# Performance work log

Hardware: AMD Instinct MI355X
Metric: run time of the kernel (lower is better)

Reference implementation:

```python
import jax, jax.numpy as jnp
import numpy as np

K = 16  # neighbors

def setup_inputs() -> dict:
    key = jax.random.key(0)
    x = jax.random.normal(key, (2, 8192, 64), dtype=jnp.float32)
    return {"x": x}

def reference(x):
    # pairwise squared euclidean distance: ||xi||^2 - 2 xi.xj + ||xj||^2
    b, n, d = x.shape
    x_inner = -2.0 * jnp.einsum('bnd,bmd->bnm', x, x)          # (B,N,N)
    x_sq = jnp.sum(x * x, axis=-1, keepdims=True)               # (B,N,1)
    dist = x_sq + x_inner + jnp.swapaxes(x_sq, 1, 2)            # (B,N,N)
    # torch.topk(-dist, k) -> largest of -dist == k nearest neighbors
    _, nn_idx = jax.lax.top_k(-dist, K)                         # (B,N,K) int32
    center_idx = jnp.broadcast_to(jnp.arange(n, dtype=nn_idx.dtype)[None, :, None], (b, n, K))
    return jnp.stack((nn_idx, center_idx), axis=0)              # (2,B,N,K)
```

## Files before the change

### kernel.cpp

```cpp
#include <hip/hip_runtime.h>
#include <stdint.h>

constexpr int N_    = 8192;
constexpr int D_    = 64;
constexpr int K_    = 16;
constexpr int NQ    = 16384;
constexpr int MS    = 8;
constexpr int CAPB  = 40;

typedef __attribute__((ext_vector_type(8))) short bf16x8;
typedef __attribute__((ext_vector_type(4))) float f32x4;

template<int JN>
__device__ __forceinline__ void topk_insertf(float (&key)[JN], float nk) {
    if (nk < key[JN - 1]) {
        bool c[JN];
#pragma unroll
        for (int j = 0; j < JN; ++j) c[j] = nk < key[j];
#pragma unroll
        for (int j = JN - 1; j >= 1; --j)
            key[j] = c[j - 1] ? key[j - 1] : (c[j] ? nk : key[j]);
        key[0] = c[0] ? nk : key[0];
    }
}

__device__ __forceinline__ unsigned short bf16_rne(float f) {
    uint32_t u = __float_as_uint(f);
    return (unsigned short)((u + 0x7FFFu + ((u >> 16) & 1u)) >> 16);
}

__global__ void __launch_bounds__(256) split_k(const float* __restrict__ x,
                                               unsigned short* __restrict__ xh,
                                               float* __restrict__ nrm,
                                               float* __restrict__ eres) {
    const int t = blockIdx.x * 256 + (int)threadIdx.x;
    const int row = t >> 4, seg = t & 15;
    const float4 v = reinterpret_cast<const float4*>(x)[t];
    float f[4] = {v.x, v.y, v.z, v.w};
    unsigned short h[4];
    float sq = 0.f, esq = 0.f;
#pragma unroll
    for (int j = 0; j < 4; ++j) {
        sq = fmaf(f[j], f[j], sq);
        h[j] = bf16_rne(f[j]);
        float hf = __uint_as_float((uint32_t)h[j] << 16);
        float r  = f[j] - hf;
        esq = fmaf(r, r, esq);
    }
    sq  += __shfl_xor(sq, 1, 16);  sq  += __shfl_xor(sq, 2, 16);
    sq  += __shfl_xor(sq, 4, 16);  sq  += __shfl_xor(sq, 8, 16);
    esq += __shfl_xor(esq, 1, 16); esq += __shfl_xor(esq, 2, 16);
    esq += __shfl_xor(esq, 4, 16); esq += __shfl_xor(esq, 8, 16);
    if (seg == 0) { nrm[row] = sq; eres[row] = sqrtf(esq); }
    ushort4 hv = {h[0], h[1], h[2], h[3]};
    reinterpret_cast<ushort4*>(xh)[t] = hv;
}

__global__ void __launch_bounds__(256) red_k(const float* __restrict__ nrm,
                                             const float* __restrict__ eres,
                                             float* __restrict__ EH) {
    __shared__ float mbuf[8];
    const int b = (int)blockIdx.x, tid = (int)threadIdx.x;
    float mn = 0.f, me = 0.f;
    for (int i = tid; i < N_; i += 256) {
        mn = fmaxf(mn, nrm[b * N_ + i]);
        me = fmaxf(me, eres[b * N_ + i]);
    }
#pragma unroll
    for (int s = 1; s < 64; s <<= 1) {
        mn = fmaxf(mn, __shfl_xor(mn, s, 64));
        me = fmaxf(me, __shfl_xor(me, s, 64));
    }
    const int w = tid >> 6;
    if ((tid & 63) == 0) { mbuf[w * 2] = mn; mbuf[w * 2 + 1] = me; }
    __syncthreads();
    if (tid == 0) {
        for (int i = 1; i < 4; ++i) {
            mn = fmaxf(mn, mbuf[i * 2]); me = fmaxf(me, mbuf[i * 2 + 1]);
        }
        EH[b * 2]     = sqrtf(mn) * 1.0002f + 1e-6f;
        EH[b * 2 + 1] = me * 1.0002f + 1e-7f;
    }
}

__global__ void __launch_bounds__(256, 4) tau_p(const unsigned short* __restrict__ xh,
                                                const float* __restrict__ nrm,
                                                float* __restrict__ part) {
    __shared__ alignas(16) float nrmS[512];
    const int tid = (int)threadIdx.x;
    const int bid = (int)blockIdx.x;
    const int qt  = bid >> 2, sh = bid & 3;
    const int q0g = qt * 128;
    const int b   = q0g >> 13;
    const int q0l = q0g & (N_ - 1);
    const int s0  = sh * 512;
    const unsigned short* __restrict__ xhb = xh + (size_t)b * N_ * D_;
    const float* __restrict__ nb = nrm + b * N_;
    const int w = tid >> 6, lane = tid & 63;
    const int wq = w >> 1, wm = w & 1;
    const int l15 = lane & 15, quad = lane >> 4;

    if (tid < 128) *(float4*)(nrmS + tid * 4) = *(const float4*)(nb + s0 + tid * 4);

    bf16x8 Af[2][4];
#pragma unroll
    for (int half = 0; half < 2; ++half) {
        const int eo = (half * 4 + quad) * 8;
#pragma unroll
        for (int tm = 0; tm < 4; ++tm)
            Af[half][tm] = *(const bf16x8*)(xhb + (size_t)(q0l + wq * 64 + tm * 16 + l15) * D_ + eo);
    }
    float lad[16];
#pragma unroll
    for (int j = 0; j < 16; ++j) lad[j] = __builtin_inff();
    __syncthreads();

    for (int mc = 0; mc < 8; ++mc) {
        const unsigned short* Bbase = xhb + (size_t)(s0 + mc * 64) * D_;
        bf16x8 Bf[2][2];
#pragma unroll
        for (int half = 0; half < 2; ++half) {
            const int eo = (half * 4 + quad) * 8;
#pragma unroll
            for (int tn = 0; tn < 2; ++tn)
                Bf[half][tn] = *(const bf16x8*)(Bbase + (size_t)(wm * 32 + tn * 16 + l15) * D_ + eo);
        }
        f32x4 acc[4][2] = {};
#pragma unroll
        for (int half = 0; half < 2; ++half)
#pragma unroll
            for (int tm = 0; tm < 4; ++tm)
#pragma unroll
                for (int tn = 0; tn < 2; ++tn)
                    acc[tm][tn] = __builtin_amdgcn_mfma_f32_16x16x32_bf16(Af[half][tm], Bf[half][tn], acc[tm][tn], 0, 0, 0);
#pragma unroll
        for (int tn = 0; tn < 2; ++tn) {
            const float nm = nrmS[mc * 64 + wm * 32 + tn * 16 + l15];
#pragma unroll
            for (int tm = 0; tm < 4; ++tm)
#pragma unroll
                for (int reg = 0; reg < 4; ++reg)
                    lad[tm * 4 + reg] = fminf(lad[tm * 4 + reg],
                                              fmaf(-2.f, acc[tm][tn][reg], nm));
        }
    }
#pragma unroll
    for (int tm = 0; tm < 4; ++tm)
#pragma unroll
        for (int reg = 0; reg < 4; ++reg) {
            const int q = q0g + wq * 64 + tm * 16 + quad * 4 + reg;
            part[(size_t)q * 128 + sh * 32 + wm * 16 + l15] = lad[tm * 4 + reg];
        }
}

__global__ void __launch_bounds__(64) tau_m(const float* __restrict__ part,
                                            const float* __restrict__ nrm,
                                            const float* __restrict__ eres,
                                            const float* __restrict__ EH,
                                            float* __restrict__ tau) {
    const int q = blockIdx.x * 64 + (int)threadIdx.x;
    const int b = q >> 13;
    const float4* p = reinterpret_cast<const float4*>(part + (size_t)q * 128);
    float key[K_];
#pragma unroll
    for (int j = 0; j < K_; ++j) key[j] = __builtin_inff();
    for (int i = 0; i < 32; ++i) {
        float4 v = p[i];
        topk_insertf<K_>(key, v.x); topk_insertf<K_>(key, v.y);
        topk_insertf<K_>(key, v.z); topk_insertf<K_>(key, v.w);
    }
    const float Nmax = EH[b * 2], Emax = EH[b * 2 + 1];
    const float H = Nmax + Emax;
    const float nq = sqrtf(nrm[q]) * 1.0001f, eq = eres[q];
    tau[q] = key[15] + 4.f * (nq * Emax + eq * H) + 6e-3f;
}

__global__ void __launch_bounds__(256, 4) filter_k(const unsigned short* __restrict__ xh,
                                                   const float* __restrict__ nrm,
                                                   const float* __restrict__ tau,
                                                   unsigned short* __restrict__ cnt_pb,
                                                   unsigned short* __restrict__ buf2) {
    __shared__ alignas(16) float nrmS[1024];
    __shared__ unsigned short lists[128 * CAPB];
    __shared__ unsigned int cntL[128];
    const int tid = (int)threadIdx.x;
    const int bid = (int)blockIdx.x;
    const int b  = bid >> 9;
    const int qt = (bid >> 3) & 63;
    const int ms = bid & 7;
    const int q0 = qt * 128;
    const unsigned short* __restrict__ xhb = xh + (size_t)b * N_ * D_;
    const float* __restrict__ nb = nrm + b * N_;
    const int w = tid >> 6, lane = tid & 63;
    const int wq = w >> 1, wm = w & 1;
    const int l15 = lane & 15, quad = lane >> 4;

    *(float4*)(nrmS + tid * 4) = *(const float4*)(nb + ms * 1024 + tid * 4);
    if (tid < 128) cntL[tid] = 0;

    bf16x8 Af[2][4];
#pragma unroll
    for (int half = 0; half < 2; ++half) {
        const int eo = (half * 4 + quad) * 8;
#pragma unroll
        for (int tm = 0; tm < 4; ++tm)
            Af[half][tm] = *(const bf16x8*)(xhb + (size_t)(q0 + wq * 64 + tm * 16 + l15) * D_ + eo);
    }
    f32x4 t4v[4];
#pragma unroll
    for (int tm = 0; tm < 4; ++tm)
        t4v[tm] = *(const f32x4*)(tau + (b << 13) + q0 + wq * 64 + tm * 16 + quad * 4);
    __syncthreads();

    for (int mc = 0; mc < 16; ++mc) {
        const unsigned short* Bbase = xhb + (size_t)(ms * 1024 + mc * 64) * D_;
        bf16x8 Bf[2][2];
#pragma unroll
        for (int half = 0; half < 2; ++half) {
            const int eo = (half * 4 + quad) * 8;
#pragma unroll
            for (int tn = 0; tn < 2; ++tn)
                Bf[half][tn] = *(const bf16x8*)(Bbase + (size_t)(wm * 32 + tn * 16 + l15) * D_ + eo);
        }
        f32x4 acc[4][2] = {};
#pragma unroll
        for (int half = 0; half < 2; ++half)
#pragma unroll
            for (int tm = 0; tm < 4; ++tm)
#pragma unroll
                for (int tn = 0; tn < 2; ++tn)
                    acc[tm][tn] = __builtin_amdgcn_mfma_f32_16x16x32_bf16(Af[half][tm], Bf[half][tn], acc[tm][tn], 0, 0, 0);
#pragma unroll
        for (int tn = 0; tn < 2; ++tn) {
            const int mloc = mc * 64 + wm * 32 + tn * 16 + l15;
            const float nm = nrmS[mloc];
            const unsigned short mid = (unsigned short)(ms * 1024 + mloc);
#pragma unroll
            for (int tm = 0; tm < 4; ++tm)
#pragma unroll
                for (int reg = 0; reg < 4; ++reg) {
                    float keyf = fmaf(-2.f, acc[tm][tn][reg], nm);
                    if (keyf <= t4v[tm][reg]) {
                        int ql = wq * 64 + tm * 16 + quad * 4 + reg;
                        unsigned pos = atomicAdd(&cntL[ql], 1u);
                        if (pos < CAPB) lists[ql * CAPB + pos] = mid;
                    }
                }
        }
    }
    __syncthreads();
    if (tid < 128) {
        const int q = (b << 13) + q0 + tid;
        unsigned cn = cntL[tid]; cn = cn < CAPB ? cn : CAPB;
        cnt_pb[(size_t)q * MS + ms] = (unsigned short)cn;
        unsigned short* dst = buf2 + ((size_t)q * MS + ms) * CAPB;
        for (unsigned i = 0; i < cn; ++i) dst[i] = lists[tid * CAPB + i];
    }
}

__global__ void __launch_bounds__(256) rerank_k(const float* __restrict__ x,
                                                const unsigned short* __restrict__ cnt_pb,
                                                const unsigned short* __restrict__ buf2,
                                                int* __restrict__ out) {
    __shared__ float Qs[4 * 64];
    __shared__ unsigned short ids[4 * MS * CAPB];
    const int tid = (int)threadIdx.x;
    const int w = tid >> 6, lane = tid & 63;
    const int q = blockIdx.x * 4 + w;
    const int b = q >> 13, n = q & (N_ - 1);
    const float* __restrict__ xb = x + (size_t)b * N_ * D_;
    Qs[w * 64 + lane] = xb[(size_t)n * D_ + lane];

    int off[MS + 1]; off[0] = 0;
#pragma unroll
    for (int ms = 0; ms < MS; ++ms) {
        int c = (int)cnt_pb[(size_t)q * MS + ms]; c = c < CAPB ? c : CAPB;
        off[ms + 1] = off[ms] + c;
    }
    const int total = off[MS];
    for (int idx = lane; idx < total; idx += 64) {
        int ms = 0;
#pragma unroll
        for (int t = 1; t < MS; ++t) ms += (idx >= off[t]) ? 1 : 0;
        ids[(w * MS) * CAPB + idx] = buf2[((size_t)q * MS + ms) * CAPB + (idx - off[ms])];
    }
    __syncthreads();

    unsigned long long v = ~0ull;
    int consumed = 0;
    bool first = true;
    while (first || consumed < total) {
        const int myIdx = first ? lane : consumed + lane - 16;
        const bool take = (first || lane >= 16) && myIdx < total;
        unsigned long long nk = ~0ull;
        if (take) {
            const int id = (int)ids[(w * MS) * CAPB + myIdx];
            const float* __restrict__ crow = xb + (size_t)id * D_;
            double a0 = 0.0, a1 = 0.0, a2 = 0.0, a3 = 0.0;
#pragma unroll
            for (int j = 0; j < 16; ++j) {
                const float4 c  = *(const float4*)(crow + j * 4);
                const float4 qv = *(const float4*)(Qs + w * 64 + j * 4);
                double d0 = (double)qv.x - (double)c.x; a0 = fma(d0, d0, a0);
                double d1 = (double)qv.y - (double)c.y; a1 = fma(d1, d1, a1);
                double d2 = (double)qv.z - (double)c.z; a2 = fma(d2, d2, a2);
                double d3 = (double)qv.w - (double)c.w; a3 = fma(d3, d3, a3);
            }
            double s = (a0 + a1) + (a2 + a3);
            nk = ((unsigned long long)__double_as_longlong(s) & ~0x1FFFull) | (unsigned)id;
        }
        if (first || lane >= 16) v = nk;
#pragma unroll
        for (int k = 2; k <= 64; k <<= 1)
#pragma unroll
            for (int j = k >> 1; j > 0; j >>= 1) {
                unsigned long long o = __shfl_xor(v, j, 64);
                const bool keepmin = (((lane & k) == 0) == ((lane & j) == 0));
                unsigned long long mn = v < o ? v : o;
                unsigned long long mx = v < o ? o : v;
                v = keepmin ? mn : mx;
            }
        consumed += first ? 64 : 48;
        first = false;
    }
    if (lane < K_) {
        out[(size_t)q * K_ + lane]                   = (int)(v & 0x1FFFull);
        out[(size_t)NQ * K_ + (size_t)q * K_ + lane] = n;
    }
}

extern "C" void kernel_launch(void* const* d_in, const int* in_sizes, int n_in,
                              void* d_out, int out_size, void* d_ws, size_t ws_size,
                              hipStream_t stream) {
    const float* x = (const float*)d_in[0];
    int* out = (int*)d_out;
    char* ws = (char*)d_ws;
    float*          nrm    = (float*)ws;
    float*          tau    = (float*)(ws + (64 << 10));
    float*          eres   = (float*)(ws + (128 << 10));
    float*          EH     = (float*)(ws + (192 << 10));
    unsigned short* cnt_pb = (unsigned short*)(ws + (256 << 10));
    unsigned short* xh     = (unsigned short*)(ws + (1 << 20));
    unsigned short* buf2   = (unsigned short*)(ws + (5 << 20));
    float*          part   = (float*)(ws + (5 << 20));

    hipLaunchKernelGGL(split_k,  dim3(1024), dim3(256), 0, stream, x, xh, nrm, eres);
    hipLaunchKernelGGL(red_k,    dim3(2),    dim3(256), 0, stream, nrm, eres, EH);
    hipLaunchKernelGGL(tau_p,    dim3(512),  dim3(256), 0, stream, xh, nrm, part);
    hipLaunchKernelGGL(tau_m,    dim3(256),  dim3(64),  0, stream, part, nrm, eres, EH, tau);
    hipLaunchKernelGGL(filter_k, dim3(1024), dim3(256), 0, stream, xh, nrm, tau, cnt_pb, buf2);
    hipLaunchKernelGGL(rerank_k, dim3(4096), dim3(256), 0, stream, x, cnt_pb, buf2, out);
}
```

Baseline: 208.5 us.

## Fuse max-norm reduction into split kernel and widen tau sampling slices

Removes the separate red_k launch by computing per-block maxima inside split_k and merging them with atomicMax on float bits into a zeroed buffer; tau_m now applies the sqrt and margins. tau_p samples 6 candidate slices instead of 4, which tightens the per-query threshold tau, and the filter list capacity CAPB drops from 40 to 24 to match. This trades extra sampling work in tau_p/tau_m for fewer filter candidates and smaller shared lists. The risk is overflow of the smaller candidate lists if the threshold is not tight enough.

```diff
diff --git a/kernel.cpp b/kernel.cpp
--- a/kernel.cpp
+++ b/kernel.cpp
@@ -6,7 +6,8 @@
 constexpr int K_    = 16;
 constexpr int NQ    = 16384;
 constexpr int MS    = 8;
-constexpr int CAPB  = 40;
+constexpr int CAPB  = 24;
+constexpr int NSL   = 6;
 
 typedef __attribute__((ext_vector_type(8))) short bf16x8;
 typedef __attribute__((ext_vector_type(4))) float f32x4;
@@ -32,8 +33,11 @@
 __global__ void __launch_bounds__(256) split_k(const float* __restrict__ x,
                                                unsigned short* __restrict__ xh,
                                                float* __restrict__ nrm,
-                                               float* __restrict__ eres) {
-    const int t = blockIdx.x * 256 + (int)threadIdx.x;
+                                               float* __restrict__ eres,
+                                               unsigned int* __restrict__ EHu) {
+    __shared__ float wmax[8];
+    const int tid = (int)threadIdx.x;
+    const int t = blockIdx.x * 256 + tid;
     const int row = t >> 4, seg = t & 15;
     const float4 v = reinterpret_cast<const float4*>(x)[t];
     float f[4] = {v.x, v.y, v.z, v.w};
@@ -54,32 +58,24 @@
     if (seg == 0) { nrm[row] = sq; eres[row] = sqrtf(esq); }
     ushort4 hv = {h[0], h[1], h[2], h[3]};
     reinterpret_cast<ushort4*>(xh)[t] = hv;
-}
-
-__global__ void __launch_bounds__(256) red_k(const float* __restrict__ nrm,
-                                             const float* __restrict__ eres,
-                                             float* __restrict__ EH) {
-    __shared__ float mbuf[8];
-    const int b = (int)blockIdx.x, tid = (int)threadIdx.x;
-    float mn = 0.f, me = 0.f;
-    for (int i = tid; i < N_; i += 256) {
-        mn = fmaxf(mn, nrm[b * N_ + i]);
-        me = fmaxf(me, eres[b * N_ + i]);
-    }
+
+    float bn = (seg == 0) ? sq : 0.f, be = (seg == 0) ? esq : 0.f;
 #pragma unroll
     for (int s = 1; s < 64; s <<= 1) {
-        mn = fmaxf(mn, __shfl_xor(mn, s, 64));
-        me = fmaxf(me, __shfl_xor(me, s, 64));
+        bn = fmaxf(bn, __shfl_xor(bn, s, 64));
+        be = fmaxf(be, __shfl_xor(be, s, 64));
     }
     const int w = tid >> 6;
-    if ((tid & 63) == 0) { mbuf[w * 2] = mn; mbuf[w * 2 + 1] = me; }
+    if ((tid & 63) == 0) { wmax[w * 2] = bn; wmax[w * 2 + 1] = be; }
     __syncthreads();
     if (tid == 0) {
+#pragma unroll
         for (int i = 1; i < 4; ++i) {
-            mn = fmaxf(mn, mbuf[i * 2]); me = fmaxf(me, mbuf[i * 2 + 1]);
-        }
-        EH[b * 2]     = sqrtf(mn) * 1.0002f + 1e-6f;
-        EH[b * 2 + 1] = me * 1.0002f + 1e-7f;
+            bn = fmaxf(bn, wmax[i * 2]); be = fmaxf(be, wmax[i * 2 + 1]);
+        }
+        const int b = (int)(blockIdx.x * 16) >> 13;
+        atomicMax(&EHu[b * 2],     __float_as_uint(bn));
+        atomicMax(&EHu[b * 2 + 1], __float_as_uint(be));
     }
 }
 
@@ -89,7 +85,7 @@
     __shared__ alignas(16) float nrmS[512];
     const int tid = (int)threadIdx.x;
     const int bid = (int)blockIdx.x;
-    const int qt  = bid >> 2, sh = bid & 3;
+    const int qt  = bid / NSL, sh = bid % NSL;
     const int q0g = qt * 128;
     const int b   = q0g >> 13;
     const int q0l = q0g & (N_ - 1);
@@ -149,27 +145,28 @@
 #pragma unroll
         for (int reg = 0; reg < 4; ++reg) {
             const int q = q0g + wq * 64 + tm * 16 + quad * 4 + reg;
-            part[(size_t)q * 128 + sh * 32 + wm * 16 + l15] = lad[tm * 4 + reg];
+            part[(size_t)q * 192 + sh * 32 + wm * 16 + l15] = lad[tm * 4 + reg];
         }
 }
 
 __global__ void __launch_bounds__(64) tau_m(const float* __restrict__ part,
                                             const float* __restrict__ nrm,
                                             const float* __restrict__ eres,
-                                            const float* __restrict__ EH,
+                                            const unsigned int* __restrict__ EHu,
                                             float* __restrict__ tau) {
     const int q = blockIdx.x * 64 + (int)threadIdx.x;
     const int b = q >> 13;
-    const float4* p = reinterpret_cast<const float4*>(part + (size_t)q * 128);
+    const float4* p = reinterpret_cast<const float4*>(part + (size_t)q * 192);
     float key[K_];
 #pragma unroll
     for (int j = 0; j < K_; ++j) key[j] = __builtin_inff();
-    for (int i = 0; i < 32; ++i) {
+    for (int i = 0; i < 48; ++i) {
         float4 v = p[i];
         topk_insertf<K_>(key, v.x); topk_insertf<K_>(key, v.y);
         topk_insertf<K_>(key, v.z); topk_insertf<K_>(key, v.w);
     }
-    const float Nmax = EH[b * 2], Emax = EH[b * 2 + 1];
+    const float Nmax = sqrtf(__uint_as_float(EHu[b * 2]))     * 1.0002f + 1e-6f;
+    const float Emax = sqrtf(__uint_as_float(EHu[b * 2 + 1])) * 1.0002f + 1e-7f;
     const float H = Nmax + Emax;
     const float nq = sqrtf(nrm[q]) * 1.0001f, eq = eres[q];
     tau[q] = key[15] + 4.f * (nq * Emax + eq * H) + 6e-3f;
@@ -338,16 +335,16 @@
     float*          nrm    = (float*)ws;
     float*          tau    = (float*)(ws + (64 << 10));
     float*          eres   = (float*)(ws + (128 << 10));
-    float*          EH     = (float*)(ws + (192 << 10));
+    unsigned int*   EHu    = (unsigned int*)(ws + (192 << 10));
     unsigned short* cnt_pb = (unsigned short*)(ws + (256 << 10));
     unsigned short* xh     = (unsigned short*)(ws + (1 << 20));
     unsigned short* buf2   = (unsigned short*)(ws + (5 << 20));
     float*          part   = (float*)(ws + (5 << 20));
 
-    hipLaunchKernelGGL(split_k,  dim3(1024), dim3(256), 0, stream, x, xh, nrm, eres);
-    hipLaunchKernelGGL(red_k,    dim3(2),    dim3(256), 0, stream, nrm, eres, EH);
-    hipLaunchKernelGGL(tau_p,    dim3(512),  dim3(256), 0, stream, xh, nrm, part);
-    hipLaunchKernelGGL(tau_m,    dim3(256),  dim3(64),  0, stream, part, nrm, eres, EH, tau);
-    hipLaunchKernelGGL(filter_k, dim3(1024), dim3(256), 0, stream, xh, nrm, tau, cnt_pb, buf2);
-    hipLaunchKernelGGL(rerank_k, dim3(4096), dim3(256), 0, stream, x, cnt_pb, buf2, out);
-}
+    hipMemsetAsync(EHu, 0, 16, stream);
+    hipLaunchKernelGGL(split_k,  dim3(1024),      dim3(256), 0, stream, x, xh, nrm, eres, EHu);
+    hipLaunchKernelGGL(tau_p,    dim3(128 * NSL), dim3(256), 0, stream, xh, nrm, part);
+    hipLaunchKernelGGL(tau_m,    dim3(256),       dim3(64),  0, stream, part, nrm, eres, EHu, tau);
+    hipLaunchKernelGGL(filter_k, dim3(1024),      dim3(256), 0, stream, xh, nrm, tau, cnt_pb, buf2);
+    hipLaunchKernelGGL(rerank_k, dim3(4096),      dim3(256), 0, stream, x, cnt_pb, buf2, out);
+}
```

New measurement: 215.2 us. +3.2%, slower.
